# Optimization experiments

Measured on AMD Instinct MI355X. Metric: run time of the kernel, lower is better.

Reference implementation:

```python
import jax, jax.numpy as jnp
import numpy as np


def _gcn_conv(x, src, dst, norm, W, b, n_nodes):
    # PyG GCNConv: transform then normalized scatter-add aggregation.
    h = x @ W                                        # [N, F_out]
    msg = h[src] * norm[:, None]                     # [E+N, F_out] gather
    out = jax.ops.segment_sum(msg, dst, num_segments=n_nodes)  # scatter-add
    return out + b


def setup_inputs() -> dict:
    key = jax.random.key(0)
    ks = jax.random.split(key, 8)
    N, E, F_in, H, C = 100000, 1000000, 128, 64, 40
    x = jax.random.normal(ks[0], (N, F_in), dtype=jnp.float32)
    edge_index = jax.random.randint(ks[1], (2, E), 0, N, dtype=jnp.int64)
    W1 = jax.random.normal(ks[2], (F_in, H), dtype=jnp.float32) * (1.0 / np.sqrt(F_in))
    b1 = jnp.zeros((H,), jnp.float32)
    W2 = jax.random.normal(ks[3], (H, H), dtype=jnp.float32) * (1.0 / np.sqrt(H))
    b2 = jnp.zeros((H,), jnp.float32)
    Wc = jax.random.normal(ks[4], (H, C), dtype=jnp.float32) * (1.0 / np.sqrt(H))
    bc = jnp.zeros((C,), jnp.float32)
    return {"x": x, "edge_index": edge_index, "W1": W1, "b1": b1,
            "W2": W2, "b2": b2, "Wc": Wc, "bc": bc}


def reference(x, edge_index, W1, b1, W2, b2, Wc, bc):
    n_nodes = x.shape[0]
    # Add self loops (GCNConv default), symmetric normalization.
    loop = jnp.arange(n_nodes, dtype=edge_index.dtype)
    src = jnp.concatenate([edge_index[0], loop])
    dst = jnp.concatenate([edge_index[1], loop])
    deg = jax.ops.segment_sum(jnp.ones_like(dst, jnp.float32), dst,
                              num_segments=n_nodes)
    dinv = jnp.where(deg > 0, jax.lax.rsqrt(jnp.maximum(deg, 1.0)), 0.0)
    norm = dinv[src] * dinv[dst]                     # [E+N]

    h = jax.nn.relu(_gcn_conv(x, src, dst, norm, W1, b1, n_nodes))
    # dropout: identity (inference / training=False)
    h = jax.nn.relu(_gcn_conv(h, src, dst, norm, W2, b2, n_nodes))
    return h @ Wc + bc                               # [N, out_dim]
```

## Files before the change

kernel.cpp:

```cpp
#include <hip/hip_runtime.h>
#include <hip/hip_fp16.h>


#define BUCKET_BITS  8
#define BUCKET_NODES 256
#define MAXB 512
#define CAP  8192
#define OFF_MASK 0x3FFFFF

union H8 { uint4 u; __half h[8]; };
union H4 { uint2 u; __half h[4]; };

__global__ void zero_kernel(int* __restrict__ p, int n) {
    int i = blockIdx.x * blockDim.x + threadIdx.x;
    if (i < n) p[i] = 0;
}

__global__ __launch_bounds__(256) void bucket_fill_kernel(const int* __restrict__ src,
                                                          const int* __restrict__ dst,
                                                          int* __restrict__ bucketCursor,
                                                          unsigned int* __restrict__ bucketArr,
                                                          int E, int NB) {
    __shared__ int lcnt[MAXB];
    for (int i = threadIdx.x; i < NB; i += 256) lcnt[i] = 0;
    __syncthreads();
    const int base = blockIdx.x * 4096;
#pragma unroll
    for (int k = 0; k < 16; ++k) {
        int e = base + k * 256 + threadIdx.x;
        if (e < E) atomicAdd(&lcnt[dst[e] >> BUCKET_BITS], 1);
    }
    __syncthreads();
    for (int i = threadIdx.x; i < NB; i += 256) {
        int c = lcnt[i];
        if (c) lcnt[i] = i * CAP + atomicAdd(&bucketCursor[i], c);
    }
    __syncthreads();
#pragma unroll
    for (int k = 0; k < 16; ++k) {
        int e = base + k * 256 + threadIdx.x;
        if (e < E) {
            int d = dst[e];
            int s = src[e];
            int pos = atomicAdd(&lcnt[d >> BUCKET_BITS], 1);
            bucketArr[pos] = ((unsigned)(d & (BUCKET_NODES - 1)) << 24) | (unsigned)s;
        }
    }
}

__global__ __launch_bounds__(256) void node_count_kernel(const unsigned int* __restrict__ bucketArr,
                                                         const int* __restrict__ bucketCursor,
                                                         unsigned int* __restrict__ nodeInfo,
                                                         float* __restrict__ dinv, int N) {
    __shared__ int cnt[BUCKET_NODES];
    __shared__ int scn[BUCKET_NODES];
    const int t = threadIdx.x;
    cnt[t] = 0;
    __syncthreads();
    const int b  = blockIdx.x;
    const int e0 = b * CAP;
    const int e1 = e0 + bucketCursor[b];
    for (int e = e0 + t; e < e1; e += 256)
        atomicAdd(&cnt[bucketArr[e] >> 24], 1);
    __syncthreads();
    int v = cnt[t];
    scn[t] = v;
    __syncthreads();
    for (int off = 1; off < 256; off <<= 1) {
        int u = (t >= off) ? scn[t - off] : 0;
        __syncthreads();
        scn[t] += u;
        __syncthreads();
    }
    int excl = scn[t] - v;
    int node = b * BUCKET_NODES + t;
    if (node < N) {
        nodeInfo[node] = ((unsigned)v << 22) | (unsigned)(e0 + excl);
        dinv[node]     = rsqrtf((float)(v + 1));
    }
}

__global__ __launch_bounds__(256) void adj_fill_kernel(const unsigned int* __restrict__ bucketArr,
                                                       const int* __restrict__ bucketCursor,
                                                       const unsigned int* __restrict__ nodeInfo,
                                                       const float* __restrict__ dinv,
                                                       int2* __restrict__ adj, int N) {
    __shared__ int cur[BUCKET_NODES];
    const int t = threadIdx.x;
    const int b = blockIdx.x;
    const int node = b * BUCKET_NODES + t;
    cur[t] = (node < N) ? (int)(nodeInfo[node] & OFF_MASK) : 0;
    __syncthreads();
    const int e0 = b * CAP;
    const int e1 = e0 + bucketCursor[b];
    for (int e = e0 + t; e < e1; e += 256) {
        unsigned int entry = bucketArr[e];
        int local = entry >> 24;
        int s     = entry & 0xFFFFFF;
        int pos   = atomicAdd(&cur[local], 1);
        adj[pos]  = make_int2(s, __float_as_int(dinv[s]));
    }
}

template <int K, int NOUT, bool BIAS, bool AHALF, bool OHALF>
__global__ __launch_bounds__(256) void gemm_tiled(const void* __restrict__ Av,
                                                  const float* __restrict__ W,
                                                  const float* __restrict__ bias,
                                                  void* __restrict__ outv, int M) {
    constexpr int KS  = 64;
    constexpr int NST = K / KS;
    __shared__ float At[64 * 66];
    __shared__ float Wt[K * 64];

    for (int i = threadIdx.x; i < K * 64; i += 256) {
        if (NOUT == 64) {
            Wt[i] = W[i];
        } else {
            int k = i >> 6, c = i & 63;
            Wt[i] = (c < NOUT) ? W[k * NOUT + c] : 0.f;
        }
    }

    const int tc   = threadIdx.x & 15;
    const int tr   = threadIdx.x >> 4;
    const int row0 = blockIdx.x * 64;

    float acc[4][4] = {};

    for (int st = 0; st < NST; ++st) {
        __syncthreads();
        if (AHALF) {
            const __half* Ah = (const __half*)Av;
            int g = threadIdx.x;
#pragma unroll
            for (int i = 0; i < 2; ++i, g += 256) {
                int r  = g >> 3;
                int kc = (g & 7) << 3;
                int grow = row0 + r;
                if (grow > M - 1) grow = M - 1;
                H8 v;
                v.u = *(const uint4*)(Ah + (size_t)grow * K + st * KS + kc);
                float* p = &At[r * 66 + kc];
#pragma unroll
                for (int j = 0; j < 8; ++j) p[j] = __half2float(v.h[j]);
            }
        } else {
            const float* Af = (const float*)Av;
            int g = threadIdx.x;
#pragma unroll
            for (int i = 0; i < 4; ++i, g += 256) {
                int r  = g >> 4;
                int kc = (g & 15) << 2;
                int grow = row0 + r;
                if (grow > M - 1) grow = M - 1;
                float4 v = *(const float4*)(Af + (size_t)grow * K + st * KS + kc);
                float* p = &At[r * 66 + kc];
                p[0] = v.x; p[1] = v.y; p[2] = v.z; p[3] = v.w;
            }
        }
        __syncthreads();

        const float* a0p = &At[(tr * 4 + 0) * 66];
        const float* a1p = &At[(tr * 4 + 1) * 66];
        const float* a2p = &At[(tr * 4 + 2) * 66];
        const float* a3p = &At[(tr * 4 + 3) * 66];
        const float* wp  = &Wt[st * KS * 64 + tc * 4];
#pragma unroll 8
        for (int k = 0; k < KS; ++k) {
            float a0 = a0p[k];
            float a1 = a1p[k];
            float a2 = a2p[k];
            float a3 = a3p[k];
            float4 w = *(const float4*)(wp + k * 64);
            acc[0][0] += a0 * w.x; acc[0][1] += a0 * w.y; acc[0][2] += a0 * w.z; acc[0][3] += a0 * w.w;
            acc[1][0] += a1 * w.x; acc[1][1] += a1 * w.y; acc[1][2] += a1 * w.z; acc[1][3] += a1 * w.w;
            acc[2][0] += a2 * w.x; acc[2][1] += a2 * w.y; acc[2][2] += a2 * w.z; acc[2][3] += a2 * w.w;
            acc[3][0] += a3 * w.x; acc[3][1] += a3 * w.y; acc[3][2] += a3 * w.z; acc[3][3] += a3 * w.w;
        }
    }

    if (NOUT < 64 && tc * 4 >= NOUT) return;
    float4 bb = {0.f, 0.f, 0.f, 0.f};
    if (BIAS) bb = *(const float4*)(bias + tc * 4);
#pragma unroll
    for (int j = 0; j < 4; ++j) {
        int row = row0 + tr * 4 + j;
        if (row >= M) break;
        float vx = acc[j][0] + bb.x;
        float vy = acc[j][1] + bb.y;
        float vz = acc[j][2] + bb.z;
        float vw = acc[j][3] + bb.w;
        if (OHALF) {
            __half* oh = (__half*)outv;
            H4 v;
            v.h[0] = __float2half(vx); v.h[1] = __float2half(vy);
            v.h[2] = __float2half(vz); v.h[3] = __float2half(vw);
            *(uint2*)(oh + (size_t)row * NOUT + tc * 4) = v.u;
        } else {
            float4 v = {vx, vy, vz, vw};
            *(float4*)((float*)outv + (size_t)row * NOUT + tc * 4) = v;
        }
    }
}

__global__ __launch_bounds__(256) void gather_kernel(const __half* __restrict__ h,
                                                     const unsigned int* __restrict__ nodeInfo,
                                                     const int2* __restrict__ adj,
                                                     const float* __restrict__ dinv,
                                                     const float* __restrict__ bias,
                                                     __half* __restrict__ out, int N) {
    const int node = blockIdx.x * 32 + (threadIdx.x >> 3);
    const int o    = (threadIdx.x >> 3) & 7;
    const int l    = threadIdx.x & 7;
    if (node >= N) return;

    const unsigned info = nodeInfo[node];
    const int start = (int)(info & OFF_MASK);
    const int end   = start + (int)(info >> 22);
    const float di  = dinv[node];

    float acc[8];
    {
        H8 sv;
        sv.u = *(const uint4*)(h + (size_t)node * 64 + l * 8);
#pragma unroll
        for (int k = 0; k < 8; ++k) acc[k] = __half2float(sv.h[k]) * di;
    }

    for (int base = start; ; base += 8) {
        bool active = base < end;
        if (__ballot(active) == 0ull) break;
        int m = 0;
        int   sidx = 0;
        float sw   = 0.f;
        if (active) {
            m = min(8, end - base);
            if (l < m) {
                int2 pr = adj[base + l];
                sidx = pr.x;
                sw   = __int_as_float(pr.y);
            }
        }
#pragma unroll
        for (int j = 0; j < 8; ++j) {
            if (j < m) {
                int   s = __shfl(sidx, (o << 3) | j);
                float w = __shfl(sw,   (o << 3) | j);
                H8 rv;
                rv.u = *(const uint4*)(h + (size_t)s * 64 + l * 8);
#pragma unroll
                for (int k = 0; k < 8; ++k) acc[k] += __half2float(rv.h[k]) * w;
            }
        }
    }

    H8 ov;
#pragma unroll
    for (int k = 0; k < 8; ++k) {
        float v = acc[k] * di + bias[l * 8 + k];
        ov.h[k] = __float2half(v > 0.f ? v : 0.f);
    }
    *(uint4*)(out + (size_t)node * 64 + l * 8) = ov.u;
}

extern "C" void kernel_launch(void* const* d_in, const int* in_sizes, int n_in,
                              void* d_out, int out_size, void* d_ws, size_t ws_size,
                              hipStream_t stream) {
    const float* x  = (const float*)d_in[0];
    const int*   ei = (const int*)d_in[1];
    const float* W1 = (const float*)d_in[2];
    const float* b1 = (const float*)d_in[3];
    const float* W2 = (const float*)d_in[4];
    const float* b2 = (const float*)d_in[5];
    const float* Wc = (const float*)d_in[6];
    const float* bc = (const float*)d_in[7];

    const int N = in_sizes[0] / 128;
    const int E = in_sizes[1] / 2;
    const int* src = ei;
    const int* dst = ei + E;

    const int NB = (N + BUCKET_NODES - 1) >> BUCKET_BITS;
    const int EB = (E + 4095) / 4096;

    char* w = (char*)d_ws;
    auto alloc = [&](size_t bytes) { char* p = w; w += (bytes + 255) & ~(size_t)255; return p; };
    int*          bucketCursor = (int*)alloc((size_t)NB * 4);
    unsigned int* bucketArr    = (unsigned int*)alloc((size_t)NB * CAP * 4);
    unsigned int* nodeInfo     = (unsigned int*)alloc((size_t)N * 4);
    int2*         adj          = (int2*)alloc((size_t)NB * CAP * 8);
    float*        dinv         = (float*)alloc((size_t)N * 4);
    __half*       bufA         = (__half*)alloc((size_t)N * 64 * 2);
    __half*       bufB         = (__half*)alloc((size_t)N * 64 * 2);

    dim3 blk(256);
    const int nblkG = (N + 63) / 64;
    const int nblkV = (N + 31) / 32;

    zero_kernel<<<(NB + 255) / 256, blk, 0, stream>>>(bucketCursor, NB);
    bucket_fill_kernel<<<EB, blk, 0, stream>>>(src, dst, bucketCursor, bucketArr, E, NB);
    node_count_kernel<<<NB, blk, 0, stream>>>(bucketArr, bucketCursor, nodeInfo, dinv, N);
    adj_fill_kernel<<<NB, blk, 0, stream>>>(bucketArr, bucketCursor, nodeInfo, dinv, adj, N);

    gemm_tiled<128, 64, false, false, true><<<nblkG, blk, 0, stream>>>(x, W1, nullptr, bufA, N);
    gather_kernel<<<nblkV, blk, 0, stream>>>(bufA, nodeInfo, adj, dinv, b1, bufB, N);

    gemm_tiled<64, 64, false, true, true><<<nblkG, blk, 0, stream>>>(bufB, W2, nullptr, bufA, N);
    gather_kernel<<<nblkV, blk, 0, stream>>>(bufA, nodeInfo, adj, dinv, b2, bufB, N);

    gemm_tiled<64, 40, true, true, false><<<nblkG, blk, 0, stream>>>(bufB, Wc, bc, d_out, N);
}
```

Before: 246.4 us.

## Fold source-degree scaling into GEMM epilogue and shrink adjacency to indices

After: 239.5 us. 2.8% less time.

```diff
diff --git a/kernel.cpp b/kernel.cpp
--- a/kernel.cpp
+++ b/kernel.cpp
@@ -22,13 +22,19 @@
                                                           unsigned int* __restrict__ bucketArr,
                                                           int E, int NB) {
     __shared__ int lcnt[MAXB];
+    __shared__ int dcache[4096];
     for (int i = threadIdx.x; i < NB; i += 256) lcnt[i] = 0;
     __syncthreads();
     const int base = blockIdx.x * 4096;
 #pragma unroll
     for (int k = 0; k < 16; ++k) {
-        int e = base + k * 256 + threadIdx.x;
-        if (e < E) atomicAdd(&lcnt[dst[e] >> BUCKET_BITS], 1);
+        int idx = k * 256 + threadIdx.x;
+        int e = base + idx;
+        if (e < E) {
+            int d = dst[e];
+            dcache[idx] = d;
+            atomicAdd(&lcnt[d >> BUCKET_BITS], 1);
+        }
     }
     __syncthreads();
     for (int i = threadIdx.x; i < NB; i += 256) {
@@ -38,9 +44,10 @@
     __syncthreads();
 #pragma unroll
     for (int k = 0; k < 16; ++k) {
-        int e = base + k * 256 + threadIdx.x;
+        int idx = k * 256 + threadIdx.x;
+        int e = base + idx;
         if (e < E) {
-            int d = dst[e];
+            int d = dcache[idx];
             int s = src[e];
             int pos = atomicAdd(&lcnt[d >> BUCKET_BITS], 1);
             bucketArr[pos] = ((unsigned)(d & (BUCKET_NODES - 1)) << 24) | (unsigned)s;
@@ -48,16 +55,18 @@
     }
 }
 
-__global__ __launch_bounds__(256) void node_count_kernel(const unsigned int* __restrict__ bucketArr,
-                                                         const int* __restrict__ bucketCursor,
-                                                         unsigned int* __restrict__ nodeInfo,
-                                                         float* __restrict__ dinv, int N) {
+__global__ __launch_bounds__(256) void node_sort_kernel(const unsigned int* __restrict__ bucketArr,
+                                                        const int* __restrict__ bucketCursor,
+                                                        unsigned int* __restrict__ nodeInfo,
+                                                        float* __restrict__ dinv,
+                                                        unsigned int* __restrict__ adj, int N) {
     __shared__ int cnt[BUCKET_NODES];
     __shared__ int scn[BUCKET_NODES];
+    __shared__ int cur[BUCKET_NODES];
     const int t = threadIdx.x;
+    const int b = blockIdx.x;
     cnt[t] = 0;
     __syncthreads();
-    const int b  = blockIdx.x;
     const int e0 = b * CAP;
     const int e1 = e0 + bucketCursor[b];
     for (int e = e0 + t; e < e1; e += 256)
@@ -72,40 +81,26 @@
         scn[t] += u;
         __syncthreads();
     }
-    int excl = scn[t] - v;
-    int node = b * BUCKET_NODES + t;
+    const int excl = scn[t] - v;
+    const int node = b * BUCKET_NODES + t;
     if (node < N) {
         nodeInfo[node] = ((unsigned)v << 22) | (unsigned)(e0 + excl);
         dinv[node]     = rsqrtf((float)(v + 1));
     }
-}
-
-__global__ __launch_bounds__(256) void adj_fill_kernel(const unsigned int* __restrict__ bucketArr,
-                                                       const int* __restrict__ bucketCursor,
-                                                       const unsigned int* __restrict__ nodeInfo,
-                                                       const float* __restrict__ dinv,
-                                                       int2* __restrict__ adj, int N) {
-    __shared__ int cur[BUCKET_NODES];
-    const int t = threadIdx.x;
-    const int b = blockIdx.x;
-    const int node = b * BUCKET_NODES + t;
-    cur[t] = (node < N) ? (int)(nodeInfo[node] & OFF_MASK) : 0;
-    __syncthreads();
-    const int e0 = b * CAP;
-    const int e1 = e0 + bucketCursor[b];
+    cur[t] = e0 + excl;
+    __syncthreads();
     for (int e = e0 + t; e < e1; e += 256) {
         unsigned int entry = bucketArr[e];
-        int local = entry >> 24;
-        int s     = entry & 0xFFFFFF;
-        int pos   = atomicAdd(&cur[local], 1);
-        adj[pos]  = make_int2(s, __float_as_int(dinv[s]));
-    }
-}
-
-template <int K, int NOUT, bool BIAS, bool AHALF, bool OHALF>
+        int pos = atomicAdd(&cur[entry >> 24], 1);
+        adj[pos] = entry & 0xFFFFFF;
+    }
+}
+
+template <int K, int NOUT, bool BIAS, bool AHALF, bool OHALF, bool SCALE>
 __global__ __launch_bounds__(256) void gemm_tiled(const void* __restrict__ Av,
                                                   const float* __restrict__ W,
                                                   const float* __restrict__ bias,
+                                                  const float* __restrict__ dscale,
                                                   void* __restrict__ outv, int M) {
     constexpr int KS  = 64;
     constexpr int NST = K / KS;
@@ -186,10 +181,11 @@
     for (int j = 0; j < 4; ++j) {
         int row = row0 + tr * 4 + j;
         if (row >= M) break;
-        float vx = acc[j][0] + bb.x;
-        float vy = acc[j][1] + bb.y;
-        float vz = acc[j][2] + bb.z;
-        float vw = acc[j][3] + bb.w;
+        float sc = SCALE ? dscale[row] : 1.f;
+        float vx = acc[j][0] * sc + bb.x;
+        float vy = acc[j][1] * sc + bb.y;
+        float vz = acc[j][2] * sc + bb.z;
+        float vw = acc[j][3] * sc + bb.w;
         if (OHALF) {
             __half* oh = (__half*)outv;
             H4 v;
@@ -205,7 +201,7 @@
 
 __global__ __launch_bounds__(256) void gather_kernel(const __half* __restrict__ h,
                                                      const unsigned int* __restrict__ nodeInfo,
-                                                     const int2* __restrict__ adj,
+                                                     const unsigned int* __restrict__ adj,
                                                      const float* __restrict__ dinv,
                                                      const float* __restrict__ bias,
                                                      __half* __restrict__ out, int N) {
@@ -224,40 +220,37 @@
         H8 sv;
         sv.u = *(const uint4*)(h + (size_t)node * 64 + l * 8);
 #pragma unroll
-        for (int k = 0; k < 8; ++k) acc[k] = __half2float(sv.h[k]) * di;
+        for (int k = 0; k < 8; ++k) acc[k] = __half2float(sv.h[k]);
     }
 
     for (int base = start; ; base += 8) {
         bool active = base < end;
         if (__ballot(active) == 0ull) break;
         int m = 0;
-        int   sidx = 0;
-        float sw   = 0.f;
+        int sidx = 0;
         if (active) {
             m = min(8, end - base);
-            if (l < m) {
-                int2 pr = adj[base + l];
-                sidx = pr.x;
-                sw   = __int_as_float(pr.y);
-            }
+            if (l < m) sidx = (int)adj[base + l];
         }
 #pragma unroll
         for (int j = 0; j < 8; ++j) {
             if (j < m) {
-                int   s = __shfl(sidx, (o << 3) | j);
-                float w = __shfl(sw,   (o << 3) | j);
+                int s = __shfl(sidx, (o << 3) | j);
                 H8 rv;
                 rv.u = *(const uint4*)(h + (size_t)s * 64 + l * 8);
 #pragma unroll
-                for (int k = 0; k < 8; ++k) acc[k] += __half2float(rv.h[k]) * w;
+                for (int k = 0; k < 8; ++k) acc[k] += __half2float(rv.h[k]);
             }
         }
     }
 
+    const float4 b0 = *(const float4*)(bias + l * 8);
+    const float4 b1 = *(const float4*)(bias + l * 8 + 4);
+    const float bb[8] = {b0.x, b0.y, b0.z, b0.w, b1.x, b1.y, b1.z, b1.w};
     H8 ov;
 #pragma unroll
     for (int k = 0; k < 8; ++k) {
-        float v = acc[k] * di + bias[l * 8 + k];
+        float v = acc[k] * di + bb[k];
         ov.h[k] = __float2half(v > 0.f ? v : 0.f);
     }
     *(uint4*)(out + (size_t)node * 64 + l * 8) = ov.u;
@@ -288,7 +281,7 @@
     int*          bucketCursor = (int*)alloc((size_t)NB * 4);
     unsigned int* bucketArr    = (unsigned int*)alloc((size_t)NB * CAP * 4);
     unsigned int* nodeInfo     = (unsigned int*)alloc((size_t)N * 4);
-    int2*         adj          = (int2*)alloc((size_t)NB * CAP * 8);
+    unsigned int* adj          = (unsigned int*)alloc((size_t)NB * CAP * 4);
     float*        dinv         = (float*)alloc((size_t)N * 4);
     __half*       bufA         = (__half*)alloc((size_t)N * 64 * 2);
     __half*       bufB         = (__half*)alloc((size_t)N * 64 * 2);
@@ -299,14 +292,13 @@
 
     zero_kernel<<<(NB + 255) / 256, blk, 0, stream>>>(bucketCursor, NB);
     bucket_fill_kernel<<<EB, blk, 0, stream>>>(src, dst, bucketCursor, bucketArr, E, NB);
-    node_count_kernel<<<NB, blk, 0, stream>>>(bucketArr, bucketCursor, nodeInfo, dinv, N);
-    adj_fill_kernel<<<NB, blk, 0, stream>>>(bucketArr, bucketCursor, nodeInfo, dinv, adj, N);
-
-    gemm_tiled<128, 64, false, false, true><<<nblkG, blk, 0, stream>>>(x, W1, nullptr, bufA, N);
+    node_sort_kernel<<<NB, blk, 0, stream>>>(bucketArr, bucketCursor, nodeInfo, dinv, adj, N);
+
+    gemm_tiled<128, 64, false, false, true, true><<<nblkG, blk, 0, stream>>>(x, W1, nullptr, dinv, bufA, N);
     gather_kernel<<<nblkV, blk, 0, stream>>>(bufA, nodeInfo, adj, dinv, b1, bufB, N);
 
-    gemm_tiled<64, 64, false, true, true><<<nblkG, blk, 0, stream>>>(bufB, W2, nullptr, bufA, N);
+    gemm_tiled<64, 64, false, true, true, true><<<nblkG, blk, 0, stream>>>(bufB, W2, nullptr, dinv, bufA, N);
     gather_kernel<<<nblkV, blk, 0, stream>>>(bufA, nodeInfo, adj, dinv, b2, bufB, N);
 
-    gemm_tiled<64, 40, true, true, false><<<nblkG, blk, 0, stream>>>(bufB, Wc, bc, d_out, N);
-}
+    gemm_tiled<64, 40, true, true, false, false><<<nblkG, blk, 0, stream>>>(bufB, Wc, bc, nullptr, d_out, N);
+}
```
